# Performance work log

Hardware: AMD Instinct MI355X
Metric: run time of the kernel (lower is better)

Reference implementation:

```python
import jax, jax.numpy as jnp
import numpy as np

B, C, H, W = 16, 256, 64, 64
E = 8           # num_experts
TOPK = 2
HID = int(C * 2.0)  # hidden_mult = 2.0 -> 512


def setup_inputs() -> dict:
    key = jax.random.key(0)
    ks = jax.random.split(key, 6)
    x = jax.random.normal(ks[0], (B, C, H, W), dtype=jnp.float32)
    Wr = jax.random.normal(ks[1], (C, E), dtype=jnp.float32) * 0.02
    br = jnp.zeros((E,), dtype=jnp.float32)
    W1 = jax.random.normal(ks[2], (E, C, HID), dtype=jnp.float32) * 0.02
    b1 = jnp.zeros((E, HID), dtype=jnp.float32)
    W2 = jax.random.normal(ks[3], (E, HID, C), dtype=jnp.float32) * 0.02
    b2 = jnp.zeros((E, C), dtype=jnp.float32)
    # nn.Parameter(torch.zeros(1)) in the original; use a small random value so
    scale = jax.random.normal(ks[4], (1,), dtype=jnp.float32) * 0.1
    return {"x": x, "Wr": Wr, "br": br, "W1": W1, "b1": b1,
            "W2": W2, "b2": b2, "scale": scale}


def reference(x, Wr, br, W1, b1, W2, b2, scale):
    b, c, h, w = x.shape
    tokens = jnp.transpose(x, (0, 2, 3, 1)).reshape(b, h * w, c)  # (B, T, C)
    logits = tokens @ Wr + br                                      # (B, T, E)
    topv, topi = jax.lax.top_k(logits, TOPK)                       # (B, T, K)
    wts = jax.nn.softmax(topv, axis=-1)                            # (B, T, K)

    out = jnp.zeros_like(tokens)
    num_experts = Wr.shape[1]
    for e in range(num_experts):
        # combine weight for expert e: sum of routing weights where selected
        we = jnp.sum(jnp.where(topi == e, wts, 0.0), axis=-1)      # (B, T)
        hdn = jax.nn.gelu(tokens @ W1[e] + b1[e], approximate=False)
        y = hdn @ W2[e] + b2[e]                                    # (B, T, C)
        out = out + y * we[..., None]

    out = jnp.transpose(out.reshape(b, h, w, c), (0, 3, 1, 2))     # (B, C, H, W)
    return x + scale[0] * out
```

## Files before the change

### kernel.cpp

```cpp
#include <hip/hip_runtime.h>
#include <hip/hip_bf16.h>
#include <math.h>

#define HW   4096
#define CCH  256
#define NE   8
#define HID  512
#define NTOK 65536
#define PADH 260

typedef short s16x8 __attribute__((ext_vector_type(8)));
typedef float f32x4 __attribute__((ext_vector_type(4)));

__device__ __forceinline__ float fast_gelu(float v) {
    float v2 = v * v;
    float s  = v * fmaf(0.10294324f, v2, 2.3022079f);
    float e  = exp2f(-s);
    return v * __builtin_amdgcn_rcpf(1.0f + e);
}

__global__ __launch_bounds__(256) void k_transpose_cast(
    const float* __restrict__ in, __hip_bfloat16* __restrict__ out, int R, int CC)
{
    __shared__ float t[64][65];
    int tilesC = CC >> 6;
    int per = (R >> 6) * tilesC;
    int e = blockIdx.x / per, tt = blockIdx.x % per;
    int r0 = (tt / tilesC) << 6, c0 = (tt % tilesC) << 6;
    const float* ip = in + (size_t)e * R * CC;
    __hip_bfloat16* op = out + (size_t)e * R * CC;
    int lane = threadIdx.x & 63, g = threadIdx.x >> 6;
    for (int i = 0; i < 16; i++) {
        int r = i * 4 + g;
        t[r][lane] = ip[(size_t)(r0 + r) * CC + c0 + lane];
    }
    __syncthreads();
    for (int i = 0; i < 16; i++) {
        int r = i * 4 + g;
        op[(size_t)(c0 + r) * R + r0 + lane] = __float2bfloat16(t[lane][r]);
    }
}

__global__ __launch_bounds__(256) void k_router(
    const float* __restrict__ x, const float* __restrict__ Wr, const float* __restrict__ br,
    __hip_bfloat16* __restrict__ tokens, int* __restrict__ pair, float2* __restrict__ wts,
    int* __restrict__ meta )
{
    __shared__ float xt[CCH][65];
    __shared__ float wr[CCH][NE];
    __shared__ float lg[64][NE];
    __shared__ int lc[NE];
    int tid = threadIdx.x;
    int n0 = blockIdx.x * 64;
    int b = n0 >> 12, p0 = n0 & 4095;
    const float* xb = x + (size_t)b * CCH * HW + p0;
    for (int i = tid; i < CCH * NE; i += 256) ((float*)wr)[i] = Wr[i];
    if (tid < NE) lc[tid] = 0;
    int lane = tid & 63, wv = tid >> 6;
    for (int i = 0; i < 64; i++) {
        int c = i * 4 + wv;
        xt[c][lane] = xb[(size_t)c * HW + lane];
    }
    __syncthreads();
    float a0 = br[2 * wv], a1 = br[2 * wv + 1];
    for (int c = 0; c < CCH; c++) {
        float xv = xt[c][lane];
        a0 = fmaf(xv, wr[c][2 * wv], a0);
        a1 = fmaf(xv, wr[c][2 * wv + 1], a1);
    }
    lg[lane][2 * wv] = a0;
    lg[lane][2 * wv + 1] = a1;
    __syncthreads();
    if (wv == 0) {
        float v0 = -1e30f, v1 = -1e30f; int i0 = 0, i1 = 0;
        for (int e = 0; e < NE; e++) {
            float l = lg[lane][e];
            if (l > v0)      { v1 = v0; i1 = i0; v0 = l; i0 = e; }
            else if (l > v1) { v1 = l; i1 = e; }
        }
        float e1 = expf(v1 - v0);
        float s = 1.0f + e1;
        wts[n0 + lane] = make_float2(1.0f / s, e1 / s);
        pair[n0 + lane] = i0 | (i1 << 8);
        atomicAdd(&lc[i0], 1);
        atomicAdd(&lc[i1], 1);
    }
    __syncthreads();
    if (tid < NE && lc[tid] > 0) atomicAdd(&meta[tid], lc[tid]);
    for (int r = 0; r < 64; r++)
        tokens[(size_t)(n0 + r) * CCH + tid] = __float2bfloat16(xt[tid][r]);
}

__global__ void k_scan(int* meta)
{
    if (threadIdx.x == 0) {
        int off = 0, toff = 0;
        for (int e = 0; e < NE; e++) {
            meta[16 + e] = off;
            meta[25 + e] = toff;
            int c = meta[e];
            off += c;
            toff += (c + 63) >> 6;
        }
        meta[24] = off;
        meta[33] = toff;
        meta[34] = toff;
    }
}

__global__ __launch_bounds__(256) void k_scatter(
    const int* __restrict__ pair, const float2* __restrict__ wts,
    int* __restrict__ meta, int* __restrict__ assign_tok, float* __restrict__ assign_w,
    int2* __restrict__ tok_slots)
{
    __shared__ int lcount[NE];
    __shared__ int lbase[NE];
    int tid = threadIdx.x;
    int n = blockIdx.x * 256 + tid;
    if (tid < NE) lcount[tid] = 0;
    __syncthreads();
    int pr = pair[n];
    int e0 = pr & 0xff, e1 = (pr >> 8) & 0xff;
    int p0 = atomicAdd(&lcount[e0], 1);
    int p1 = atomicAdd(&lcount[e1], 1);
    __syncthreads();
    if (tid < NE) lbase[tid] = atomicAdd(&meta[8 + tid], lcount[tid]);
    __syncthreads();
    float2 w = wts[n];
    int s0 = meta[16 + e0] + lbase[e0] + p0;
    int s1 = meta[16 + e1] + lbase[e1] + p1;
    assign_tok[s0] = n; assign_w[s0] = w.x;
    assign_tok[s1] = n; assign_w[s1] = w.y;
    tok_slots[n] = make_int2(s0, s1);
}

__global__ __launch_bounds__(512, 4) void k_expert(
    const __hip_bfloat16* __restrict__ tokens,
    const __hip_bfloat16* __restrict__ w1t,
    const __hip_bfloat16* __restrict__ w2t,
    const float* __restrict__ b1, const float* __restrict__ b2,
    const int* __restrict__ meta,
    const int* __restrict__ assign_tok, const float* __restrict__ assign_w,
    __hip_bfloat16* __restrict__ ybuf)
{
    __shared__ __align__(16) __hip_bfloat16 Af[64 * 256];
    __shared__ __align__(16) __hip_bfloat16 Hs[64 * PADH];
    __shared__ float wrow[64];
    __shared__ int trow[64];

    int total = meta[34];
    int bid = blockIdx.x;
    if (bid >= total) return;
    int e = 0;
    while (e < 7 && bid >= meta[25 + e + 1]) e++;
    int tile = bid - meta[25 + e];
    int cnt = meta[e];
    int r0 = tile << 6;
    int abase = meta[16 + e] + r0;
    int nrows = cnt - r0; if (nrows > 64) nrows = 64;

    int tid = threadIdx.x;
    if (tid < 64) {
        if (tid < nrows) { trow[tid] = assign_tok[abase + tid]; wrow[tid] = assign_w[abase + tid]; }
        else             { trow[tid] = 0; wrow[tid] = 0.0f; }
    }
    __syncthreads();

    {
        uint4* dst = (uint4*)Af;
#pragma unroll
        for (int j = 0; j < 4; j++) {
            int row = j * 16 + (tid & 15);
            int chunk = (tid >> 4) & 31;
            dst[j * 512 + tid] = ((const uint4*)(tokens + (size_t)trow[row] * CCH))[chunk];
        }
    }

    int lane = tid & 63, wv = tid >> 6;
    int quad = lane >> 4, l15 = lane & 15;

    const __hip_bfloat16* w1e = w1t + (size_t)e * HID * CCH;
    const __hip_bfloat16* w2e = w2t + (size_t)e * CCH * HID;
    const float* b1e = b1 + e * HID;
    const float* b2e = b2 + e * CCH;

    const s16x8* apb = (const s16x8*)Af + quad * 16 + l15;

    const s16x8* bq0h[2]; const s16x8* bq1h[2];
#pragma unroll
    for (int h = 0; h < 2; h++) {
        int c0 = h * 256 + wv * 32;
        bq0h[h] = (const s16x8*)(w1e + (size_t)(c0)      * CCH + (size_t)l15 * CCH + quad * 8);
        bq1h[h] = (const s16x8*)(w1e + (size_t)(c0 + 16) * CCH + (size_t)l15 * CCH + quad * 8);
    }

    f32x4 oacc[4][2];
#pragma unroll
    for (int i = 0; i < 4; i++)
#pragma unroll
        for (int j = 0; j < 2; j++) oacc[i][j] = (f32x4){0.f, 0.f, 0.f, 0.f};

    s16x8 bf0 = bq0h[0][0], bf1 = bq1h[0][0];
    float ob0 = b2e[wv * 32 + l15];
    float ob1 = b2e[wv * 32 + 16 + l15];

    __syncthreads();

#pragma unroll
    for (int h = 0; h < 2; h++) {
        const s16x8* bq0 = bq0h[h];
        const s16x8* bq1 = bq1h[h];

        f32x4 hacc[4][2];
#pragma unroll
        for (int i = 0; i < 4; i++)
#pragma unroll
            for (int j = 0; j < 2; j++) hacc[i][j] = (f32x4){0.f, 0.f, 0.f, 0.f};

#pragma unroll
        for (int kk = 0; kk < 8; kk++) {
            s16x8 bn0, bn1;
            if (kk < 7) { bn0 = bq0[(kk + 1) * 4]; bn1 = bq1[(kk + 1) * 4]; }
            s16x8 af[4];
#pragma unroll
            for (int mt = 0; mt < 4; mt++) af[mt] = apb[mt * 512 + kk * 4 * 16];
            __builtin_amdgcn_s_setprio(1);
#pragma unroll
            for (int mt = 0; mt < 4; mt++) {
                hacc[mt][0] = __builtin_amdgcn_mfma_f32_16x16x32_bf16(af[mt], bf0, hacc[mt][0], 0, 0, 0);
                hacc[mt][1] = __builtin_amdgcn_mfma_f32_16x16x32_bf16(af[mt], bf1, hacc[mt][1], 0, 0, 0);
            }
            __builtin_amdgcn_s_setprio(0);
            bf0 = bn0; bf1 = bn1;
        }

        const s16x8* b2q0 = (const s16x8*)(w2e + (size_t)(wv * 32      + l15) * HID + h * 256 + quad * 8);
        const s16x8* b2q1 = (const s16x8*)(w2e + (size_t)(wv * 32 + 16 + l15) * HID + h * 256 + quad * 8);
        s16x8 cf0 = b2q0[0], cf1 = b2q1[0];
        float biasA = b1e[h * 256 + wv * 32 + l15];
        float biasB = b1e[h * 256 + wv * 32 + 16 + l15];
        if (h == 0) { bf0 = bq0h[1][0]; bf1 = bq1h[1][0]; }

        __syncthreads();
#pragma unroll
        for (int nt = 0; nt < 2; nt++) {
            int cl = wv * 32 + nt * 16 + l15;
            float bias = nt ? biasB : biasA;
#pragma unroll
            for (int mt = 0; mt < 4; mt++)
#pragma unroll
                for (int r = 0; r < 4; r++) {
                    int row = mt * 16 + quad * 4 + r;
                    float v = hacc[mt][nt][r] + bias;
                    Hs[row * PADH + cl] = __float2bfloat16(fast_gelu(v));
                }
        }
        __syncthreads();

#pragma unroll
        for (int kk = 0; kk < 8; kk++) {
            s16x8 cn0, cn1;
            if (kk < 7) { cn0 = b2q0[(kk + 1) * 4]; cn1 = b2q1[(kk + 1) * 4]; }
            s16x8 hf[4];
#pragma unroll
            for (int mt = 0; mt < 4; mt++)
                hf[mt] = *(const s16x8*)(Hs + (mt * 16 + l15) * PADH + kk * 32 + quad * 8);
            __builtin_amdgcn_s_setprio(1);
#pragma unroll
            for (int mt = 0; mt < 4; mt++) {
                oacc[mt][0] = __builtin_amdgcn_mfma_f32_16x16x32_bf16(hf[mt], cf0, oacc[mt][0], 0, 0, 0);
                oacc[mt][1] = __builtin_amdgcn_mfma_f32_16x16x32_bf16(hf[mt], cf1, oacc[mt][1], 0, 0, 0);
            }
            __builtin_amdgcn_s_setprio(0);
            cf0 = cn0; cf1 = cn1;
        }
        if (h == 0) __syncthreads();
    }

#pragma unroll
    for (int nt = 0; nt < 2; nt++) {
        int cc = wv * 32 + nt * 16 + l15;
        float bias = nt ? ob1 : ob0;
#pragma unroll
        for (int mt = 0; mt < 4; mt++) {
#pragma unroll
            for (int r = 0; r < 4; r++) {
                int row = mt * 16 + quad * 4 + r;
                if (row < nrows) {
                    float v = (oacc[mt][nt][r] + bias) * wrow[row];
                    ybuf[(size_t)(abase + row) * CCH + cc] = __float2bfloat16(v);
                }
            }
        }
    }
}

__global__ __launch_bounds__(256) void k_combine(
    const float* __restrict__ x, const __hip_bfloat16* __restrict__ ybuf,
    const int2* __restrict__ tok_slots, const float* __restrict__ scale,
    float* __restrict__ out)
{
    __shared__ float moe[CCH][65];
    __shared__ int2 slots[64];
    int tid = threadIdx.x;
    int n0 = blockIdx.x * 64;
    if (tid < 64) slots[tid] = tok_slots[n0 + tid];
    __syncthreads();
    for (int r = 0; r < 64; r++) {
        int2 s = slots[r];
        float y = __bfloat162float(ybuf[(size_t)s.x * CCH + tid]) +
                  __bfloat162float(ybuf[(size_t)s.y * CCH + tid]);
        moe[tid][r] = y;
    }
    __syncthreads();
    float sc = scale[0];
    int b = n0 >> 12, p0 = n0 & 4095;
    const float* xb = x + (size_t)b * CCH * HW + p0;
    float* ob = out + (size_t)b * CCH * HW + p0;
    int lane = tid & 63, wv = tid >> 6;
    for (int i = 0; i < 64; i++) {
        int c = i * 4 + wv;
        ob[(size_t)c * HW + lane] = xb[(size_t)c * HW + lane] + sc * moe[c][lane];
    }
}

extern "C" void kernel_launch(void* const* d_in, const int* in_sizes, int n_in,
                              void* d_out, int out_size, void* d_ws, size_t ws_size,
                              hipStream_t stream)
{
    const float* x     = (const float*)d_in[0];
    const float* Wr    = (const float*)d_in[1];
    const float* br    = (const float*)d_in[2];
    const float* W1    = (const float*)d_in[3];
    const float* b1    = (const float*)d_in[4];
    const float* W2    = (const float*)d_in[5];
    const float* b2    = (const float*)d_in[6];
    const float* scale = (const float*)d_in[7];
    float* out = (float*)d_out;

    char* ws = (char*)d_ws;
    __hip_bfloat16* tokens = (__hip_bfloat16*)(ws);
    __hip_bfloat16* w1t    = (__hip_bfloat16*)(ws + 33554432);
    __hip_bfloat16* w2t    = (__hip_bfloat16*)(ws + 35651584);
    __hip_bfloat16* ybuf   = (__hip_bfloat16*)(ws + 37748736);
    int*    assign_tok = (int*)   (ws + 104857600);
    float*  assign_w   = (float*) (ws + 105381888);
    int2*   tok_slots  = (int2*)  (ws + 105906176);
    int*    pair       = (int*)   (ws + 106430464);
    float2* wts        = (float2*)(ws + 106692608);
    int*    meta       = (int*)   (ws + 107216896);

    hipMemsetAsync(meta, 0, 64, stream);
    k_transpose_cast<<<256, 256, 0, stream>>>(W1, w1t, 256, 512);
    k_transpose_cast<<<256, 256, 0, stream>>>(W2, w2t, 512, 256);
    k_router<<<1024, 256, 0, stream>>>(x, Wr, br, tokens, pair, wts, meta);
    k_scan<<<1, 64, 0, stream>>>(meta);
    k_scatter<<<256, 256, 0, stream>>>(pair, wts, meta, assign_tok, assign_w, tok_slots);
    k_expert<<<2056, 512, 0, stream>>>(tokens, w1t, w2t, b1, b2, meta,
                                       assign_tok, assign_w, ybuf);
    k_combine<<<1024, 256, 0, stream>>>(x, ybuf, tok_slots, scale, out);
}
```

Measured before the change: 344.0 us.

## Merge weight transposes and scan into neighbors, vectorize router and combine loads

Folds the two weight transpose kernels and the meta memset into one launch, and moves the expert-offset prefix scan into every scatter block so the single-thread scan kernel disappears. The router's x tile load now uses float2 accesses. The combine kernel uses 32-token blocks with 16-byte bf16 gathers and float4 reads and writes of x and out. The aim is fewer launches and wider memory transactions in the memory-bound phases, at the cost of every scatter block re-reading the eight expert counts.

```diff
diff --git a/kernel.cpp b/kernel.cpp
--- a/kernel.cpp
+++ b/kernel.cpp
@@ -11,6 +11,7 @@
 
 typedef short s16x8 __attribute__((ext_vector_type(8)));
 typedef float f32x4 __attribute__((ext_vector_type(4)));
+typedef unsigned short u16x8 __attribute__((ext_vector_type(8)));
 
 __device__ __forceinline__ float fast_gelu(float v) {
     float v2 = v * v;
@@ -19,13 +20,24 @@
     return v * __builtin_amdgcn_rcpf(1.0f + e);
 }
 
-__global__ __launch_bounds__(256) void k_transpose_cast(
-    const float* __restrict__ in, __hip_bfloat16* __restrict__ out, int R, int CC)
+__device__ __forceinline__ float bfbits2f(unsigned short h) {
+    return __uint_as_float(((unsigned)h) << 16);
+}
+
+__global__ __launch_bounds__(256) void k_transpose_both(
+    const float* __restrict__ W1, const float* __restrict__ W2,
+    __hip_bfloat16* __restrict__ w1t, __hip_bfloat16* __restrict__ w2t,
+    int* __restrict__ meta)
 {
     __shared__ float t[64][65];
+    if (blockIdx.x == 0 && threadIdx.x < 16) meta[threadIdx.x] = 0;
+    int bb = blockIdx.x;
+    const float* in; __hip_bfloat16* out; int R, CC;
+    if (bb < 256) { in = W1; out = w1t; R = 256; CC = 512; }
+    else          { in = W2; out = w2t; R = 512; CC = 256; bb -= 256; }
     int tilesC = CC >> 6;
     int per = (R >> 6) * tilesC;
-    int e = blockIdx.x / per, tt = blockIdx.x % per;
+    int e = bb / per, tt = bb % per;
     int r0 = (tt / tilesC) << 6, c0 = (tt % tilesC) << 6;
     const float* ip = in + (size_t)e * R * CC;
     __hip_bfloat16* op = out + (size_t)e * R * CC;
@@ -46,7 +58,7 @@
     __hip_bfloat16* __restrict__ tokens, int* __restrict__ pair, float2* __restrict__ wts,
     int* __restrict__ meta )
 {
-    __shared__ float xt[CCH][65];
+    __shared__ float xt[CCH][66];
     __shared__ float wr[CCH][NE];
     __shared__ float lg[64][NE];
     __shared__ int lc[NE];
@@ -57,9 +69,13 @@
     for (int i = tid; i < CCH * NE; i += 256) ((float*)wr)[i] = Wr[i];
     if (tid < NE) lc[tid] = 0;
     int lane = tid & 63, wv = tid >> 6;
-    for (int i = 0; i < 64; i++) {
-        int c = i * 4 + wv;
-        xt[c][lane] = xb[(size_t)c * HW + lane];
+    {
+        int j2 = tid & 31, cg = tid >> 5;
+        for (int i = 0; i < 32; i++) {
+            int c = cg + 8 * i;
+            float2 v = *(const float2*)(xb + (size_t)c * HW + 2 * j2);
+            *(float2*)&xt[c][2 * j2] = v;
+        }
     }
     __syncthreads();
     float a0 = br[2 * wv], a1 = br[2 * wv + 1];
@@ -91,23 +107,6 @@
         tokens[(size_t)(n0 + r) * CCH + tid] = __float2bfloat16(xt[tid][r]);
 }
 
-__global__ void k_scan(int* meta)
-{
-    if (threadIdx.x == 0) {
-        int off = 0, toff = 0;
-        for (int e = 0; e < NE; e++) {
-            meta[16 + e] = off;
-            meta[25 + e] = toff;
-            int c = meta[e];
-            off += c;
-            toff += (c + 63) >> 6;
-        }
-        meta[24] = off;
-        meta[33] = toff;
-        meta[34] = toff;
-    }
-}
-
 __global__ __launch_bounds__(256) void k_scatter(
     const int* __restrict__ pair, const float2* __restrict__ wts,
     int* __restrict__ meta, int* __restrict__ assign_tok, float* __restrict__ assign_w,
@@ -115,6 +114,7 @@
 {
     __shared__ int lcount[NE];
     __shared__ int lbase[NE];
+    __shared__ int soff[NE];
     int tid = threadIdx.x;
     int n = blockIdx.x * 256 + tid;
     if (tid < NE) lcount[tid] = 0;
@@ -124,11 +124,22 @@
     int p0 = atomicAdd(&lcount[e0], 1);
     int p1 = atomicAdd(&lcount[e1], 1);
     __syncthreads();
+    if (tid == 0) {
+        int off = 0, toff = 0;
+        for (int ee = 0; ee < NE; ee++) {
+            soff[ee] = off;
+            int c = meta[ee];
+            if (blockIdx.x == 0) { meta[16 + ee] = off; meta[25 + ee] = toff; }
+            off += c;
+            toff += (c + 63) >> 6;
+        }
+        if (blockIdx.x == 0) { meta[24] = off; meta[33] = toff; meta[34] = toff; }
+    }
     if (tid < NE) lbase[tid] = atomicAdd(&meta[8 + tid], lcount[tid]);
     __syncthreads();
     float2 w = wts[n];
-    int s0 = meta[16 + e0] + lbase[e0] + p0;
-    int s1 = meta[16 + e1] + lbase[e1] + p1;
+    int s0 = soff[e0] + lbase[e0] + p0;
+    int s1 = soff[e1] + lbase[e1] + p1;
     assign_tok[s0] = n; assign_w[s0] = w.x;
     assign_tok[s1] = n; assign_w[s1] = w.y;
     tok_slots[n] = make_int2(s0, s1);
@@ -300,27 +311,42 @@
     const int2* __restrict__ tok_slots, const float* __restrict__ scale,
     float* __restrict__ out)
 {
-    __shared__ float moe[CCH][65];
-    __shared__ int2 slots[64];
+    __shared__ float moe[CCH][33];
+    __shared__ int2 slots[32];
     int tid = threadIdx.x;
-    int n0 = blockIdx.x * 64;
-    if (tid < 64) slots[tid] = tok_slots[n0 + tid];
-    __syncthreads();
-    for (int r = 0; r < 64; r++) {
+    int n0 = blockIdx.x * 32;
+    if (tid < 32) slots[tid] = tok_slots[n0 + tid];
+    __syncthreads();
+#pragma unroll
+    for (int it = 0; it < 2; it++) {
+        int r = (tid >> 4) + 16 * it;
+        int g = tid & 15;
         int2 s = slots[r];
-        float y = __bfloat162float(ybuf[(size_t)s.x * CCH + tid]) +
-                  __bfloat162float(ybuf[(size_t)s.y * CCH + tid]);
-        moe[tid][r] = y;
+        const u16x8* px = (const u16x8*)(ybuf + (size_t)s.x * CCH + 16 * g);
+        const u16x8* py = (const u16x8*)(ybuf + (size_t)s.y * CCH + 16 * g);
+        u16x8 ax0 = px[0], ax1 = px[1], ay0 = py[0], ay1 = py[1];
+#pragma unroll
+        for (int k = 0; k < 8; k++) {
+            moe[16 * g + k][r]     = bfbits2f(ax0[k]) + bfbits2f(ay0[k]);
+            moe[16 * g + 8 + k][r] = bfbits2f(ax1[k]) + bfbits2f(ay1[k]);
+        }
     }
     __syncthreads();
     float sc = scale[0];
     int b = n0 >> 12, p0 = n0 & 4095;
     const float* xb = x + (size_t)b * CCH * HW + p0;
     float* ob = out + (size_t)b * CCH * HW + p0;
-    int lane = tid & 63, wv = tid >> 6;
-    for (int i = 0; i < 64; i++) {
-        int c = i * 4 + wv;
-        ob[(size_t)c * HW + lane] = xb[(size_t)c * HW + lane] + sc * moe[c][lane];
+    int j = tid & 7, cbase = tid >> 3;
+#pragma unroll
+    for (int i = 0; i < 8; i++) {
+        int c = cbase + 32 * i;
+        float4 xv = *(const float4*)(xb + (size_t)c * HW + 4 * j);
+        float4 o;
+        o.x = xv.x + sc * moe[c][4 * j];
+        o.y = xv.y + sc * moe[c][4 * j + 1];
+        o.z = xv.z + sc * moe[c][4 * j + 2];
+        o.w = xv.w + sc * moe[c][4 * j + 3];
+        *(float4*)(ob + (size_t)c * HW + 4 * j) = o;
     }
 }
 
@@ -350,13 +376,10 @@
     float2* wts        = (float2*)(ws + 106692608);
     int*    meta       = (int*)   (ws + 107216896);
 
-    hipMemsetAsync(meta, 0, 64, stream);
-    k_transpose_cast<<<256, 256, 0, stream>>>(W1, w1t, 256, 512);
-    k_transpose_cast<<<256, 256, 0, stream>>>(W2, w2t, 512, 256);
+    k_transpose_both<<<512, 256, 0, stream>>>(W1, W2, w1t, w2t, meta);
     k_router<<<1024, 256, 0, stream>>>(x, Wr, br, tokens, pair, wts, meta);
-    k_scan<<<1, 64, 0, stream>>>(meta);
     k_scatter<<<256, 256, 0, stream>>>(pair, wts, meta, assign_tok, assign_w, tok_slots);
     k_expert<<<2056, 512, 0, stream>>>(tokens, w1t, w2t, b1, b2, meta,
                                        assign_tok, assign_w, ybuf);
-    k_combine<<<1024, 256, 0, stream>>>(x, ybuf, tok_slots, scale, out);
-}
+    k_combine<<<2048, 256, 0, stream>>>(x, ybuf, tok_slots, scale, out);
+}
```

New measurement: 341.2 us. About the same (-0.8%).
